# Performance work log

Measured on AMD Instinct MI355X. Metric: run time of the kernel, lower is better.

## Reference

```python
import jax, jax.numpy as jnp
import numpy as np
import math

D = 1024
H = 16
HEAD_D = D // H  # 64
T = 2048
B = 4


def setup_inputs() -> dict:
    key = jax.random.key(0)
    k1, k2, k3 = jax.random.split(key, 3)
    x = jax.random.normal(k1, (B, T, D), dtype=jnp.float32)
    # c_attn: Linear(d, d + 2*head_d, bias=False) -> weight applied as x @ W
    w_attn = jax.random.normal(k2, (D, D + 2 * HEAD_D), dtype=jnp.float32) * (1.0 / math.sqrt(D))
    w_proj = jax.random.normal(k3, (D, D), dtype=jnp.float32) * (1.0 / math.sqrt(D))
    return {"x": x, "w_attn": w_attn, "w_proj": w_proj}


def reference(x, w_attn, w_proj):
    Bv, Tv, _ = x.shape
    qkv = x @ w_attn  # [B,T,D+2*head_d]
    q = qkv[..., :D].reshape(Bv, Tv, H, HEAD_D).transpose(0, 2, 1, 3)  # [B,H,T,hd]
    k = qkv[..., D:D + HEAD_D]        # [B,T,hd] single shared KV head
    v = qkv[..., D + HEAD_D:]         # [B,T,hd]
    scale = 1.0 / math.sqrt(HEAD_D)
    # att: [B,H,T,T], shared K broadcast over H query heads
    att = jnp.einsum('bhqd,bkd->bhqk', q, k) * scale
    causal = jnp.tril(jnp.ones((Tv, Tv), dtype=bool))  # [T,T]
    att = jnp.where(causal[None, None, :, :], att, -jnp.inf)
    att = jax.nn.softmax(att, axis=-1)
    y = jnp.einsum('bhqk,bkd->bhqd', att, v)           # [B,H,T,hd]
    y = y.transpose(0, 2, 1, 3).reshape(Bv, Tv, D)     # [B,T,D]
    return y @ w_proj
```

## Files before the change

### kernel.cpp

```cpp
#include <hip/hip_runtime.h>

typedef unsigned short u16;
typedef unsigned int u32;
typedef __attribute__((ext_vector_type(8))) short short8;
typedef __attribute__((ext_vector_type(4))) float f32x4;
typedef __attribute__((ext_vector_type(4))) u16 u16x4;

__device__ __forceinline__ u16 f2bf(float f) {
  union { float f; unsigned u; } x; x.f = f;
  unsigned r = (x.u + 0x7fffu + ((x.u >> 16) & 1u)) >> 16;
  return (u16)r;
}

__device__ __forceinline__ u16 f2bf_rna(float f) {
  union { float f; u32 u; } x; x.f = f;
  return (u16)((x.u + 0x8000u) >> 16);
}

__device__ __forceinline__ f32x4 mfma16(short8 a, short8 b, f32x4 c) {
  return __builtin_amdgcn_mfma_f32_16x16x32_bf16(a, b, c, 0, 0, 0);
}

__device__ __forceinline__ void gload16(const u16* g, u16* l) {
  __builtin_amdgcn_global_load_lds((const __attribute__((address_space(1))) void*)g,
                                   (__attribute__((address_space(3))) void*)l, 16, 0, 0);
}

__global__ __launch_bounds__(256) void prep(const float* __restrict__ w_attn,
                                            const float* __restrict__ w_proj,
                                            u16* __restrict__ wat,
                                            u16* __restrict__ wpt) {
  __shared__ float tile[32][33];
  const int bid = blockIdx.x, tid = threadIdx.x;
  const float* src; u16* dst; int C, bx, by;
  if (bid < 1152) { src = w_attn; dst = wat; C = 1152; bx = bid % 36; by = bid / 36; }
  else { int id = bid - 1152; src = w_proj; dst = wpt; C = 1024; bx = id & 31; by = id >> 5; }
  const int R = 1024;
  const int tx = tid & 31, ty = tid >> 5;
  int c = bx * 32 + tx, r0 = by * 32;
#pragma unroll
  for (int i = 0; i < 32; i += 8)
    tile[ty + i][tx] = src[(size_t)(r0 + ty + i) * C + c];
  __syncthreads();
  int oc = r0 + tx, orow0 = bx * 32;
#pragma unroll
  for (int i = 0; i < 32; i += 8)
    dst[(size_t)(orow0 + ty + i) * R + oc] = f2bf(tile[tx][ty + i]);
}

template <bool A_F32, bool C_F32, bool VT>
__global__ __launch_bounds__(256) void gemm_bt(const void* __restrict__ Ap,
                                               const u16* __restrict__ Bt,
                                               void* __restrict__ Cp,
                                               u16* __restrict__ vt,
                                               int lda, int ldb, int ldc, int K) {
  __shared__ u16 As[128 * 32];
  __shared__ u16 Bs[128 * 32];
  const int tid = threadIdx.x;
  const int wid = tid >> 6, lane = tid & 63;
  const int quad = lane >> 4, l15 = lane & 15;
  const int m0 = blockIdx.y * 128, n0 = blockIdx.x * 128;
  const int wm = (wid & 1) * 64, wn = (wid >> 1) * 64;
  const int sr = tid >> 2;
  const int sc = (tid & 3) * 8;

  f32x4 acc[4][4] = {};

  for (int k0 = 0; k0 < K; k0 += 32) {
    __syncthreads();
#pragma unroll
    for (int cch = 0; cch < 2; ++cch) {
      int row = sr + cch * 64;
      if (A_F32) {
        const float* A = (const float*)Ap;
        const f32x4* srcp = (const f32x4*)(A + (size_t)(m0 + row) * lda + k0 + sc);
        f32x4 f0 = srcp[0], f1 = srcp[1];
        short8 h;
#pragma unroll
        for (int j = 0; j < 4; ++j) { h[j] = (short)f2bf(f0[j]); h[j + 4] = (short)f2bf(f1[j]); }
        *(short8*)&As[row * 32 + sc] = h;
      } else {
        gload16((const u16*)Ap + (size_t)(m0 + row) * lda + k0 + sc, &As[wid * 512 + cch * 2048]);
      }
      gload16(Bt + (size_t)(n0 + row) * ldb + k0 + sc, &Bs[wid * 512 + cch * 2048]);
    }
    __syncthreads();
    short8 a[4], b[4];
#pragma unroll
    for (int i = 0; i < 4; ++i) a[i] = *(const short8*)&As[(wm + 16 * i + l15) * 32 + quad * 8];
#pragma unroll
    for (int j = 0; j < 4; ++j) b[j] = *(const short8*)&Bs[(wn + 16 * j + l15) * 32 + quad * 8];
#pragma unroll
    for (int i = 0; i < 4; ++i)
#pragma unroll
      for (int j = 0; j < 4; ++j)
        acc[i][j] = mfma16(a[i], b[j], acc[i][j]);
  }

#pragma unroll
  for (int i = 0; i < 4; ++i) {
#pragma unroll
    for (int j = 0; j < 4; ++j) {
      const int mrow = m0 + wm + 16 * i + quad * 4;
      const int ncol = n0 + wn + 16 * j + l15;
#pragma unroll
      for (int r = 0; r < 4; ++r) {
        float v = acc[i][j][r];
        if (C_F32) {
          ((float*)Cp)[(size_t)(mrow + r) * ldc + ncol] = v;
        } else {
          u16 hv = f2bf(v);
          ((u16*)Cp)[(size_t)(mrow + r) * ldc + ncol] = hv;
          if (VT) {
            if (ncol >= 1088) {
              int mg = mrow + r;
              int bb = mg >> 11, tt = mg & 2047;
              vt[(size_t)(bb * 64 + (ncol - 1088)) * 2048 + tt] = hv;
            }
          }
        }
      }
    }
  }
}

__global__ __launch_bounds__(256) void attn_kernel(const u16* __restrict__ qkv,
                                                   const u16* __restrict__ vt,
                                                   u16* __restrict__ y) {
  const int T = 2048, LD = 1152;
  __shared__ u16 Ks[64 * 72];
  __shared__ u16 Vts[64 * 72];
  __shared__ u16 Pw[4][2][16 * 72];

  const int bid = blockIdx.x;
  const int pr = bid >> 6;
  const int bh = bid & 63, b = bh >> 4, h = bh & 15;
  const int tid = threadIdx.x, wid = tid >> 6, lane = tid & 63;
  const int quad = lane >> 4, l15 = lane & 15;
  const int wq = wid * 32;
  const u16* qkvb = qkv + (size_t)b * T * LD;
  const u16* vtb = vt + (size_t)b * 64 * 2048;
  const int sr0 = (tid * 8) >> 6, sc0 = (tid * 8) & 63;
  const int sr1 = sr0 + 32;
  const float c1 = 0.18033688f;
  const float M = 18.0f;
  short8 ones;
#pragma unroll
  for (int j = 0; j < 8; ++j) ones[j] = (short)0x3F80;

#pragma unroll
  for (int ph = 0; ph < 2; ++ph) {
    const int qt = ph ? pr : (15 - pr);
    const int q0 = qt * 128;
    const int ktmax = 2 * qt + 2;

    short8 qreg[2][2];
#pragma unroll
    for (int jt = 0; jt < 2; ++jt)
#pragma unroll
      for (int ks = 0; ks < 2; ++ks)
        qreg[jt][ks] = *(const short8*)(qkvb + (size_t)(q0 + wq + 16 * jt + l15) * LD + h * 64 + ks * 32 + quad * 8);

    f32x4 acc[4][2] = {};
    f32x4 accs[2] = {};

    short8 kr0 = *(const short8*)(qkvb + (size_t)sr0 * LD + 1024 + sc0);
    short8 kr1 = *(const short8*)(qkvb + (size_t)sr1 * LD + 1024 + sc0);
    short8 vr0 = *(const short8*)(vtb + (size_t)sr0 * 2048 + sc0);
    short8 vr1 = *(const short8*)(vtb + (size_t)sr1 * 2048 + sc0);

    for (int kt = 0; kt < ktmax; ++kt) {
      const int kv0 = kt * 64;
      __syncthreads();
      *(short8*)&Ks[sr0 * 72 + sc0] = kr0;
      *(short8*)&Ks[sr1 * 72 + sc0] = kr1;
      *(short8*)&Vts[sr0 * 72 + sc0] = vr0;
      *(short8*)&Vts[sr1 * 72 + sc0] = vr1;
      __syncthreads();
      if (kt + 1 < ktmax) {
        const int nv0 = kv0 + 64;
        kr0 = *(const short8*)(qkvb + (size_t)(nv0 + sr0) * LD + 1024 + sc0);
        kr1 = *(const short8*)(qkvb + (size_t)(nv0 + sr1) * LD + 1024 + sc0);
        vr0 = *(const short8*)(vtb + (size_t)sr0 * 2048 + nv0 + sc0);
        vr1 = *(const short8*)(vtb + (size_t)sr1 * 2048 + nv0 + sc0);
      }
      if (kv0 > q0 + wq + 31) continue;

      f32x4 st[4][2] = {};
#pragma unroll
      for (int ks = 0; ks < 2; ++ks) {
        short8 kf[4];
#pragma unroll
        for (int i = 0; i < 4; ++i) kf[i] = *(const short8*)&Ks[(16 * i + l15) * 72 + ks * 32 + quad * 8];
#pragma unroll
        for (int i = 0; i < 4; ++i)
#pragma unroll
          for (int jt = 0; jt < 2; ++jt)
            st[i][jt] = mfma16(kf[i], qreg[jt][ks], st[i][jt]);
      }

      const bool needMask = (kv0 + 63 > q0 + wq);
#pragma unroll
      for (int jt = 0; jt < 2; ++jt) {
        u16* pw = &Pw[wid][jt][0];
        const int qg = q0 + wq + 16 * jt + l15;
#pragma unroll
        for (int i = 0; i < 4; ++i) {
          u16x4 pk;
#pragma unroll
          for (int r = 0; r < 4; ++r) {
            float p = __builtin_amdgcn_exp2f(fmaf(st[i][jt][r], c1, -M));
            if (needMask && (kv0 + 16 * i + quad * 4 + r > qg)) p = 0.f;
            pk[r] = f2bf_rna(p);
          }
          *(u16x4*)&pw[l15 * 72 + 16 * i + quad * 4] = pk;
        }
      }

#pragma unroll
      for (int ks = 0; ks < 2; ++ks) {
        short8 pf[2];
#pragma unroll
        for (int jt = 0; jt < 2; ++jt)
          pf[jt] = *(const short8*)&Pw[wid][jt][l15 * 72 + ks * 32 + quad * 8];
#pragma unroll
        for (int id = 0; id < 4; ++id) {
          short8 vf = *(const short8*)&Vts[(16 * id + l15) * 72 + ks * 32 + quad * 8];
          acc[id][0] = mfma16(vf, pf[0], acc[id][0]);
          acc[id][1] = mfma16(vf, pf[1], acc[id][1]);
        }
        accs[0] = mfma16(ones, pf[0], accs[0]);
        accs[1] = mfma16(ones, pf[1], accs[1]);
      }
    }

#pragma unroll
    for (int jt = 0; jt < 2; ++jt) {
      const float inv = 1.f / accs[jt][0];
      const int qg = q0 + wq + 16 * jt + l15;
#pragma unroll
      for (int id = 0; id < 4; ++id) {
        u16x4 o;
#pragma unroll
        for (int r = 0; r < 4; ++r) o[r] = f2bf(acc[id][jt][r] * inv);
        *(u16x4*)(y + (size_t)(b * T + qg) * 1024 + h * 64 + 16 * id + quad * 4) = o;
      }
    }
    __syncthreads();
  }
}

extern "C" void kernel_launch(void* const* d_in, const int* in_sizes, int n_in,
                              void* d_out, int out_size, void* d_ws, size_t ws_size,
                              hipStream_t stream) {
  const float* x = (const float*)d_in[0];
  const float* w_attn = (const float*)d_in[1];
  const float* w_proj = (const float*)d_in[2];
  float* out = (float*)d_out;
  char* ws = (char*)d_ws;

  u16* wat = (u16*)ws;
  u16* wpt = (u16*)(ws + 2359296);
  u16* qkv = (u16*)(ws + 4456448);
  u16* vt  = (u16*)(ws + 23330816);
  u16* y   = (u16*)(ws + 24379392);

  prep<<<dim3(2176), dim3(256), 0, stream>>>(w_attn, w_proj, wat, wpt);
  gemm_bt<true, false, true><<<dim3(9, 64), 256, 0, stream>>>(x, wat, qkv, vt, 1024, 1024, 1152, 1024);
  attn_kernel<<<dim3(512), dim3(256), 0, stream>>>(qkv, vt, y);
  gemm_bt<false, true, false><<<dim3(8, 64), 256, 0, stream>>>(y, wpt, out, nullptr, 1024, 1024, 1024, 1024);
}
```

Measured before the change: 242.8 us.

## Pre-convert x to bf16 in prep and split attention into one q-tile per block

The prep kernel now also converts x to bf16 in an extra set of blocks, so the QKV GEMM can stream A through direct global-to-LDS loads instead of converting fp32 on the fly in the main loop. The attention kernel drops the paired long/short q-tile loop and launches 1024 blocks, each handling a single q-tile, with heavy tiles scheduled first. This costs an extra round trip of x through memory and gives up the explicit load balancing of the paired tiles, in exchange for a simpler GEMM inner loop and more blocks in flight.

```diff
diff --git a/kernel.cpp b/kernel.cpp
--- a/kernel.cpp
+++ b/kernel.cpp
@@ -26,12 +26,28 @@
                                    (__attribute__((address_space(3))) void*)l, 16, 0, 0);
 }
 
-__global__ __launch_bounds__(256) void prep(const float* __restrict__ w_attn,
+__global__ __launch_bounds__(256) void prep(const float* __restrict__ x,
+                                            const float* __restrict__ w_attn,
                                             const float* __restrict__ w_proj,
+                                            u16* __restrict__ xb,
                                             u16* __restrict__ wat,
                                             u16* __restrict__ wpt) {
   __shared__ float tile[32][33];
   const int bid = blockIdx.x, tid = threadIdx.x;
+  if (bid >= 2176) {
+    const int id = bid - 2176;
+    const f32x4* src = (const f32x4*)(x + (size_t)id * 4096);
+    u16x4* dst = (u16x4*)(xb + (size_t)id * 4096);
+#pragma unroll
+    for (int c = 0; c < 4; ++c) {
+      f32x4 v = src[c * 256 + tid];
+      u16x4 o;
+#pragma unroll
+      for (int j = 0; j < 4; ++j) o[j] = f2bf(v[j]);
+      dst[c * 256 + tid] = o;
+    }
+    return;
+  }
   const float* src; u16* dst; int C, bx, by;
   if (bid < 1152) { src = w_attn; dst = wat; C = 1152; bx = bid % 36; by = bid / 36; }
   else { int id = bid - 1152; src = w_proj; dst = wpt; C = 1024; bx = id & 31; by = id >> 5; }
@@ -48,8 +64,8 @@
     dst[(size_t)(orow0 + ty + i) * R + oc] = f2bf(tile[tx][ty + i]);
 }
 
-template <bool A_F32, bool C_F32, bool VT>
-__global__ __launch_bounds__(256) void gemm_bt(const void* __restrict__ Ap,
+template <bool C_F32, bool VT>
+__global__ __launch_bounds__(256) void gemm_bt(const u16* __restrict__ A,
                                                const u16* __restrict__ Bt,
                                                void* __restrict__ Cp,
                                                u16* __restrict__ vt,
@@ -71,17 +87,7 @@
 #pragma unroll
     for (int cch = 0; cch < 2; ++cch) {
       int row = sr + cch * 64;
-      if (A_F32) {
-        const float* A = (const float*)Ap;
-        const f32x4* srcp = (const f32x4*)(A + (size_t)(m0 + row) * lda + k0 + sc);
-        f32x4 f0 = srcp[0], f1 = srcp[1];
-        short8 h;
-#pragma unroll
-        for (int j = 0; j < 4; ++j) { h[j] = (short)f2bf(f0[j]); h[j + 4] = (short)f2bf(f1[j]); }
-        *(short8*)&As[row * 32 + sc] = h;
-      } else {
-        gload16((const u16*)Ap + (size_t)(m0 + row) * lda + k0 + sc, &As[wid * 512 + cch * 2048]);
-      }
+      gload16(A + (size_t)(m0 + row) * lda + k0 + sc, &As[wid * 512 + cch * 2048]);
       gload16(Bt + (size_t)(n0 + row) * ldb + k0 + sc, &Bs[wid * 512 + cch * 2048]);
     }
     __syncthreads();
@@ -133,8 +139,9 @@
   __shared__ u16 Pw[4][2][16 * 72];
 
   const int bid = blockIdx.x;
-  const int pr = bid >> 6;
+  const int qt = 15 - (bid >> 6);
   const int bh = bid & 63, b = bh >> 4, h = bh & 15;
+  const int q0 = qt * 128;
   const int tid = threadIdx.x, wid = tid >> 6, lane = tid & 63;
   const int quad = lane >> 4, l15 = lane & 15;
   const int wq = wid * 32;
@@ -148,105 +155,98 @@
 #pragma unroll
   for (int j = 0; j < 8; ++j) ones[j] = (short)0x3F80;
 
-#pragma unroll
-  for (int ph = 0; ph < 2; ++ph) {
-    const int qt = ph ? pr : (15 - pr);
-    const int q0 = qt * 128;
-    const int ktmax = 2 * qt + 2;
-
-    short8 qreg[2][2];
-#pragma unroll
-    for (int jt = 0; jt < 2; ++jt)
-#pragma unroll
-      for (int ks = 0; ks < 2; ++ks)
-        qreg[jt][ks] = *(const short8*)(qkvb + (size_t)(q0 + wq + 16 * jt + l15) * LD + h * 64 + ks * 32 + quad * 8);
-
-    f32x4 acc[4][2] = {};
-    f32x4 accs[2] = {};
-
-    short8 kr0 = *(const short8*)(qkvb + (size_t)sr0 * LD + 1024 + sc0);
-    short8 kr1 = *(const short8*)(qkvb + (size_t)sr1 * LD + 1024 + sc0);
-    short8 vr0 = *(const short8*)(vtb + (size_t)sr0 * 2048 + sc0);
-    short8 vr1 = *(const short8*)(vtb + (size_t)sr1 * 2048 + sc0);
-
-    for (int kt = 0; kt < ktmax; ++kt) {
-      const int kv0 = kt * 64;
-      __syncthreads();
-      *(short8*)&Ks[sr0 * 72 + sc0] = kr0;
-      *(short8*)&Ks[sr1 * 72 + sc0] = kr1;
-      *(short8*)&Vts[sr0 * 72 + sc0] = vr0;
-      *(short8*)&Vts[sr1 * 72 + sc0] = vr1;
-      __syncthreads();
-      if (kt + 1 < ktmax) {
-        const int nv0 = kv0 + 64;
-        kr0 = *(const short8*)(qkvb + (size_t)(nv0 + sr0) * LD + 1024 + sc0);
-        kr1 = *(const short8*)(qkvb + (size_t)(nv0 + sr1) * LD + 1024 + sc0);
-        vr0 = *(const short8*)(vtb + (size_t)sr0 * 2048 + nv0 + sc0);
-        vr1 = *(const short8*)(vtb + (size_t)sr1 * 2048 + nv0 + sc0);
+  short8 qreg[2][2];
+#pragma unroll
+  for (int jt = 0; jt < 2; ++jt)
+#pragma unroll
+    for (int ks = 0; ks < 2; ++ks)
+      qreg[jt][ks] = *(const short8*)(qkvb + (size_t)(q0 + wq + 16 * jt + l15) * LD + h * 64 + ks * 32 + quad * 8);
+
+  f32x4 acc[4][2] = {};
+  f32x4 accs[2] = {};
+
+  short8 kr0 = *(const short8*)(qkvb + (size_t)sr0 * LD + 1024 + sc0);
+  short8 kr1 = *(const short8*)(qkvb + (size_t)sr1 * LD + 1024 + sc0);
+  short8 vr0 = *(const short8*)(vtb + (size_t)sr0 * 2048 + sc0);
+  short8 vr1 = *(const short8*)(vtb + (size_t)sr1 * 2048 + sc0);
+
+  const int ktmax = 2 * qt + 2;
+  for (int kt = 0; kt < ktmax; ++kt) {
+    const int kv0 = kt * 64;
+    __syncthreads();
+    *(short8*)&Ks[sr0 * 72 + sc0] = kr0;
+    *(short8*)&Ks[sr1 * 72 + sc0] = kr1;
+    *(short8*)&Vts[sr0 * 72 + sc0] = vr0;
+    *(short8*)&Vts[sr1 * 72 + sc0] = vr1;
+    __syncthreads();
+    if (kt + 1 < ktmax) {
+      const int nv0 = kv0 + 64;
+      kr0 = *(const short8*)(qkvb + (size_t)(nv0 + sr0) * LD + 1024 + sc0);
+      kr1 = *(const short8*)(qkvb + (size_t)(nv0 + sr1) * LD + 1024 + sc0);
+      vr0 = *(const short8*)(vtb + (size_t)sr0 * 2048 + nv0 + sc0);
+      vr1 = *(const short8*)(vtb + (size_t)sr1 * 2048 + nv0 + sc0);
+    }
+    if (kv0 > q0 + wq + 31) continue;
+
+    f32x4 st[4][2] = {};
+#pragma unroll
+    for (int ks = 0; ks < 2; ++ks) {
+      short8 kf[4];
+#pragma unroll
+      for (int i = 0; i < 4; ++i) kf[i] = *(const short8*)&Ks[(16 * i + l15) * 72 + ks * 32 + quad * 8];
+#pragma unroll
+      for (int i = 0; i < 4; ++i)
+#pragma unroll
+        for (int jt = 0; jt < 2; ++jt)
+          st[i][jt] = mfma16(kf[i], qreg[jt][ks], st[i][jt]);
+    }
+
+    const bool needMask = (kv0 + 63 > q0 + wq);
+#pragma unroll
+    for (int jt = 0; jt < 2; ++jt) {
+      u16* pw = &Pw[wid][jt][0];
+      const int qg = q0 + wq + 16 * jt + l15;
+#pragma unroll
+      for (int i = 0; i < 4; ++i) {
+        u16x4 pk;
+#pragma unroll
+        for (int r = 0; r < 4; ++r) {
+          float p = __builtin_amdgcn_exp2f(fmaf(st[i][jt][r], c1, -M));
+          if (needMask && (kv0 + 16 * i + quad * 4 + r > qg)) p = 0.f;
+          pk[r] = f2bf_rna(p);
+        }
+        *(u16x4*)&pw[l15 * 72 + 16 * i + quad * 4] = pk;
       }
-      if (kv0 > q0 + wq + 31) continue;
-
-      f32x4 st[4][2] = {};
-#pragma unroll
-      for (int ks = 0; ks < 2; ++ks) {
-        short8 kf[4];
-#pragma unroll
-        for (int i = 0; i < 4; ++i) kf[i] = *(const short8*)&Ks[(16 * i + l15) * 72 + ks * 32 + quad * 8];
-#pragma unroll
-        for (int i = 0; i < 4; ++i)
-#pragma unroll
-          for (int jt = 0; jt < 2; ++jt)
-            st[i][jt] = mfma16(kf[i], qreg[jt][ks], st[i][jt]);
+    }
+
+#pragma unroll
+    for (int ks = 0; ks < 2; ++ks) {
+      short8 pf[2];
+#pragma unroll
+      for (int jt = 0; jt < 2; ++jt)
+        pf[jt] = *(const short8*)&Pw[wid][jt][l15 * 72 + ks * 32 + quad * 8];
+#pragma unroll
+      for (int id = 0; id < 4; ++id) {
+        short8 vf = *(const short8*)&Vts[(16 * id + l15) * 72 + ks * 32 + quad * 8];
+        acc[id][0] = mfma16(vf, pf[0], acc[id][0]);
+        acc[id][1] = mfma16(vf, pf[1], acc[id][1]);
       }
-
-      const bool needMask = (kv0 + 63 > q0 + wq);
-#pragma unroll
-      for (int jt = 0; jt < 2; ++jt) {
-        u16* pw = &Pw[wid][jt][0];
-        const int qg = q0 + wq + 16 * jt + l15;
-#pragma unroll
-        for (int i = 0; i < 4; ++i) {
-          u16x4 pk;
-#pragma unroll
-          for (int r = 0; r < 4; ++r) {
-            float p = __builtin_amdgcn_exp2f(fmaf(st[i][jt][r], c1, -M));
-            if (needMask && (kv0 + 16 * i + quad * 4 + r > qg)) p = 0.f;
-            pk[r] = f2bf_rna(p);
-          }
-          *(u16x4*)&pw[l15 * 72 + 16 * i + quad * 4] = pk;
-        }
-      }
-
-#pragma unroll
-      for (int ks = 0; ks < 2; ++ks) {
-        short8 pf[2];
-#pragma unroll
-        for (int jt = 0; jt < 2; ++jt)
-          pf[jt] = *(const short8*)&Pw[wid][jt][l15 * 72 + ks * 32 + quad * 8];
-#pragma unroll
-        for (int id = 0; id < 4; ++id) {
-          short8 vf = *(const short8*)&Vts[(16 * id + l15) * 72 + ks * 32 + quad * 8];
-          acc[id][0] = mfma16(vf, pf[0], acc[id][0]);
-          acc[id][1] = mfma16(vf, pf[1], acc[id][1]);
-        }
-        accs[0] = mfma16(ones, pf[0], accs[0]);
-        accs[1] = mfma16(ones, pf[1], accs[1]);
-      }
-    }
-
-#pragma unroll
-    for (int jt = 0; jt < 2; ++jt) {
-      const float inv = 1.f / accs[jt][0];
-      const int qg = q0 + wq + 16 * jt + l15;
-#pragma unroll
-      for (int id = 0; id < 4; ++id) {
-        u16x4 o;
-#pragma unroll
-        for (int r = 0; r < 4; ++r) o[r] = f2bf(acc[id][jt][r] * inv);
-        *(u16x4*)(y + (size_t)(b * T + qg) * 1024 + h * 64 + 16 * id + quad * 4) = o;
-      }
-    }
-    __syncthreads();
+      accs[0] = mfma16(ones, pf[0], accs[0]);
+      accs[1] = mfma16(ones, pf[1], accs[1]);
+    }
+  }
+
+#pragma unroll
+  for (int jt = 0; jt < 2; ++jt) {
+    const float inv = 1.f / accs[jt][0];
+    const int qg = q0 + wq + 16 * jt + l15;
+#pragma unroll
+    for (int id = 0; id < 4; ++id) {
+      u16x4 o;
+#pragma unroll
+      for (int r = 0; r < 4; ++r) o[r] = f2bf(acc[id][jt][r] * inv);
+      *(u16x4*)(y + (size_t)(b * T + qg) * 1024 + h * 64 + 16 * id + quad * 4) = o;
+    }
   }
 }
 
@@ -261,12 +261,13 @@
 
   u16* wat = (u16*)ws;
   u16* wpt = (u16*)(ws + 2359296);
-  u16* qkv = (u16*)(ws + 4456448);
-  u16* vt  = (u16*)(ws + 23330816);
-  u16* y   = (u16*)(ws + 24379392);
-
-  prep<<<dim3(2176), dim3(256), 0, stream>>>(w_attn, w_proj, wat, wpt);
-  gemm_bt<true, false, true><<<dim3(9, 64), 256, 0, stream>>>(x, wat, qkv, vt, 1024, 1024, 1152, 1024);
-  attn_kernel<<<dim3(512), dim3(256), 0, stream>>>(qkv, vt, y);
-  gemm_bt<false, true, false><<<dim3(8, 64), 256, 0, stream>>>(y, wpt, out, nullptr, 1024, 1024, 1024, 1024);
-}
+  u16* xb  = (u16*)(ws + 4456448);
+  u16* qkv = (u16*)(ws + 21233664);
+  u16* vt  = (u16*)(ws + 40108032);
+  u16* y   = (u16*)(ws + 41156608);
+
+  prep<<<dim3(4224), dim3(256), 0, stream>>>(x, w_attn, w_proj, xb, wat, wpt);
+  gemm_bt<false, true><<<dim3(9, 64), 256, 0, stream>>>(xb, wat, qkv, vt, 1024, 1024, 1152, 1024);
+  attn_kernel<<<dim3(1024), dim3(256), 0, stream>>>(qkv, vt, y);
+  gemm_bt<true, false><<<dim3(8, 64), 256, 0, stream>>>(y, wpt, out, nullptr, 1024, 1024, 1024, 1024);
+}
```

Result: faster. 220.5 us (-9.2%).
